# Performance work log

Hardware: AMD Instinct MI355X
Metric: run time of the kernel (lower is better)

Reference implementation:

```python
import jax, jax.numpy as jnp
import numpy as np

M = 100      # max_child_num
H = 512      # node_hidden_size == node_feat_size
E = 512      # edge_dec_hidden_size
T = 4        # edge_type_num
ITERS = 2    # num_iterations (unshared)
NUM_SEM = 57


def _lin(k, i, o, s=0.02):
    kw, kb = jax.random.split(k)
    return (jax.random.normal(kw, (i, o), jnp.float32) * s,
            jax.random.normal(kb, (o,), jnp.float32) * s)


def setup_inputs() -> dict:
    key = jax.random.key(0)
    ks = jax.random.split(key, 12)
    W_parent, b_parent = _lin(ks[0], H, H * M)
    W_exists, b_exists = _lin(ks[1], H, 1)
    W_el, b_el = _lin(ks[2], 2 * H, E)
    W_ee = jax.random.normal(ks[3], (T, E), jnp.float32) * 0.02   # stacked mlp_edge_exists
    b_ee = jax.random.normal(ks[4], (T,), jnp.float32) * 0.02
    W_ne = jax.random.normal(ks[5], (ITERS, 2 * H + E + T, H), jnp.float32) * 0.02  # per-iteration node_edge_op
    b_ne = jax.random.normal(ks[6], (ITERS, H), jnp.float32) * 0.02
    W_child, b_child = _lin(ks[7], H * (ITERS + 1), H)
    W_sem, b_sem = _lin(ks[8], H, NUM_SEM)
    W_child2, b_child2 = _lin(ks[9], H, H)
    parent_feature = jax.random.normal(ks[10], (1, H), jnp.float32)
    return dict(parent_feature=parent_feature,
                W_parent=W_parent, b_parent=b_parent,
                W_exists=W_exists, b_exists=b_exists,
                W_el=W_el, b_el=b_el,
                W_ee=W_ee, b_ee=b_ee,
                W_ne=W_ne, b_ne=b_ne,
                W_child=W_child, b_child=b_child,
                W_sem=W_sem, b_sem=b_sem,
                W_child2=W_child2, b_child2=b_child2)


def reference(parent_feature, W_parent, b_parent, W_exists, b_exists,
              W_el, b_el, W_ee, b_ee, W_ne, b_ne,
              W_child, b_child, W_sem, b_sem, W_child2, b_child2):
    # parent -> M child node features
    child = jax.nn.relu(parent_feature @ W_parent + b_parent).reshape(M, H)
    exists_logits = child @ W_exists + b_exists                     # [M,1]

    # broadcast-concat pair features -> edge latents [M,M,E]
    pair = jnp.concatenate([jnp.broadcast_to(child[:, None, :], (M, M, H)),
                            jnp.broadcast_to(child[None, :, :], (M, M, H))], -1)
    edge_latents = jax.nn.relu(pair @ W_el + b_el)                  # [M,M,E]
    edge_exists_logits = jnp.einsum('ije,te->ijt', edge_latents, W_ee) + b_ee  # [M,M,T]

    # dense edge mask == torch's nonzero(edge_exists_logits>0) filtered by node existence
    node_ok = exists_logits[:, 0] > 0
    mask = (edge_exists_logits > 0) & node_ok[:, None, None] & node_ok[None, :, None]  # [M,M,T]
    maskf = mask.astype(child.dtype)[..., None]
    any_edge = mask.any()

    # per-(i,j,t) edge feature: edge_latent concat one-hot(type)*logit
    etl = edge_exists_logits[..., None] * jnp.eye(T, dtype=child.dtype)        # [M,M,T,T]
    edge_static = jnp.concatenate(
        [jnp.broadcast_to(edge_latents[:, :, None, :], (M, M, T, E)), etl], -1)  # [M,M,T,E+T]

    feats = [child]
    for it in range(ITERS):
        ne = jnp.concatenate([
            jnp.broadcast_to(child[:, None, None, :], (M, M, T, H)),   # from-node feats (gather)
            jnp.broadcast_to(child[None, :, None, :], (M, M, T, H)),   # to-node feats (gather)
            edge_static], -1)                                          # [M,M,T,2H+E+T]
        msg = jax.nn.relu(ne @ W_ne[it] + b_ne[it]) * maskf            # [M,M,T,H]
        new_child = msg.sum(axis=(1, 2))                               # scatter_add onto 'from' index
        child = jnp.where(any_edge, new_child, child)                  # torch skips update if no edges
        feats.append(child)

    hcat = jnp.concatenate(feats, axis=1)                              # [M, H*(ITERS+1)]
    h = jax.nn.relu(hcat @ W_child + b_child)
    sem_logits = h @ W_sem + b_sem
    child_out = jax.nn.relu(h @ W_child2 + b_child2)
    return (child_out[None], sem_logits[None], exists_logits[None], edge_exists_logits[None])
```

## Files before the change

kernel.cpp:

```cpp
#include <hip/hip_runtime.h>

#define M_NODES 100
#define HDIM 512
#define MH (M_NODES*HDIM)
#define WNE_IT (1540*512)

typedef __attribute__((ext_vector_type(8))) short short8v;
typedef __attribute__((ext_vector_type(4))) float float4v;

static __device__ __forceinline__ short f2b(float f) {
    union { float f; unsigned u; } v; v.f = f;
    unsigned r = (v.u + 0x7FFF + ((v.u >> 16) & 1)) >> 16;
    return (short)r;
}

__global__ void front_kernel(const float* __restrict__ W_ne, short* __restrict__ W3t,
                             const float* __restrict__ parent, const float* __restrict__ Wp,
                             float* __restrict__ partial_c, int* __restrict__ flagjc,
                             float* __restrict__ child12) {
    __shared__ float sh[32 * 33];
    int bx = blockIdx.x, t = threadIdx.x;
    if (bx == 0 && t < 101) flagjc[t] = 0;
    if (bx < 512) {
        int it = bx >> 8, rem = bx & 255, kt = rem & 15, ht = rem >> 4;
        const float* W3 = W_ne + (size_t)it * WNE_IT + 1024 * 512;
        int tx = t & 31, ty = t >> 5;
        #pragma unroll
        for (int r = 0; r < 4; ++r) {
            int k = kt * 32 + ty * 4 + r;
            sh[(ty * 4 + r) * 33 + tx] = W3[(size_t)k * 512 + ht * 32 + tx];
        }
        __syncthreads();
        #pragma unroll
        for (int r = 0; r < 4; ++r) {
            int h = ht * 32 + ty * 4 + r;
            W3t[(size_t)it * 262144 + (size_t)h * 512 + kt * 32 + tx] = f2b(sh[tx * 33 + ty * 4 + r]);
        }
    } else if (bx < 912) {
        int b = bx - 512;
        int bxx = b % 50, byy = b / 50;
        float* p = sh;
        int kc = byy * 64;
        if (t < 64) p[t] = parent[kc + t];
        __syncthreads();
        int o4 = (bxx * 256 + t) * 4;
        float4 acc = make_float4(0.f, 0.f, 0.f, 0.f);
        #pragma unroll 4
        for (int k = 0; k < 64; ++k) {
            float4 w = *(const float4*)(Wp + (size_t)(kc + k) * MH + o4);
            float pv = p[k];
            acc.x += pv * w.x; acc.y += pv * w.y; acc.z += pv * w.z; acc.w += pv * w.w;
        }
        *(float4*)(partial_c + (size_t)byy * MH + o4) = acc;
    } else {
        int id = (bx - 912) * 256 + t;
        *(float4*)(child12 + (size_t)id * 4) = make_float4(0.f, 0.f, 0.f, 0.f);
    }
}

static __device__ __forceinline__ void ks16_tree(float4 (*red)[256], int t) {
    #pragma unroll
    for (int st = 128; st >= 16; st >>= 1) {
        if (t < st) {
            #pragma unroll
            for (int r = 0; r < 4; ++r) {
                float4 a = red[r][t], b = red[r][t + st];
                a.x += b.x; a.y += b.y; a.z += b.z; a.w += b.w;
                red[r][t] = a;
            }
        }
        __syncthreads();
    }
}

__global__ __launch_bounds__(256) void
quad_ex(const float* __restrict__ partial_c, const float* __restrict__ bp,
        const float* __restrict__ Wex, const float* __restrict__ bex,
        const float* __restrict__ B0, const float* __restrict__ B1,
        const float* __restrict__ B2, const float* __restrict__ B3,
        const float* __restrict__ bias0, const float* __restrict__ bias2,
        float* __restrict__ child0, float* __restrict__ exists_out, int* __restrict__ node_ok,
        float* __restrict__ O0, float* __restrict__ O1,
        float* __restrict__ O2, float* __restrict__ O3) {
    __shared__ float As[4][512];
    __shared__ float4 red[4][256];
    int t = threadIdx.x, bx = blockIdx.x, m0 = blockIdx.y * 4;
    #pragma unroll
    for (int q2 = 0; q2 < 2; ++q2) {
        int slot = t + q2 * 256;
        int row = slot >> 7, c4 = (slot & 127) * 4;
        int gcol = (m0 + row) * 512 + c4;
        float4 s = *(const float4*)(bp + gcol);
        #pragma unroll
        for (int q = 0; q < 8; ++q) {
            float4 v = *(const float4*)(partial_c + (size_t)q * MH + gcol);
            s.x += v.x; s.y += v.y; s.z += v.z; s.w += v.w;
        }
        s.x = fmaxf(s.x, 0.f); s.y = fmaxf(s.y, 0.f);
        s.z = fmaxf(s.z, 0.f); s.w = fmaxf(s.w, 0.f);
        *(float4*)&As[row][c4] = s;
        if (bx == 0) *(float4*)(child0 + gcol) = s;
    }
    __syncthreads();
    if (bx == 0) {
        int r = t >> 6, l = t & 63;
        const float* a = &As[r][l * 8];
        const float* w = Wex + l * 8;
        float s = a[0]*w[0] + a[1]*w[1] + a[2]*w[2] + a[3]*w[3]
                + a[4]*w[4] + a[5]*w[5] + a[6]*w[6] + a[7]*w[7];
        #pragma unroll
        for (int off = 32; off; off >>= 1) s += __shfl_down(s, off);
        if (l == 0) {
            float v = s + bex[0];
            exists_out[m0 + r] = v;
            node_ok[m0 + r] = (v > 0.f) ? 1 : 0;
        }
    }
    int kq = t >> 4, g = t & 15;
    int col4 = bx * 16 + g, which = col4 >> 7, nn4 = col4 & 127;
    const float* B = (which == 0) ? B0 : (which == 1) ? B1 : (which == 2) ? B2 : B3;
    const float* bpB = B + nn4 * 4;
    float4 a0 = {0,0,0,0}, a1 = {0,0,0,0}, a2 = {0,0,0,0}, a3 = {0,0,0,0};
    int k0 = kq * 32;
    #pragma unroll 8
    for (int i = 0; i < 32; ++i) {
        int kk = k0 + i;
        float4 b = *(const float4*)(bpB + (size_t)kk * 512);
        float x0 = As[0][kk], x1 = As[1][kk], x2 = As[2][kk], x3 = As[3][kk];
        a0.x += x0*b.x; a0.y += x0*b.y; a0.z += x0*b.z; a0.w += x0*b.w;
        a1.x += x1*b.x; a1.y += x1*b.y; a1.z += x1*b.z; a1.w += x1*b.w;
        a2.x += x2*b.x; a2.y += x2*b.y; a2.z += x2*b.z; a2.w += x2*b.w;
        a3.x += x3*b.x; a3.y += x3*b.y; a3.z += x3*b.z; a3.w += x3*b.w;
    }
    red[0][t] = a0; red[1][t] = a1; red[2][t] = a2; red[3][t] = a3;
    __syncthreads();
    ks16_tree(red, t);
    if (t < 64) {
        int r2 = t >> 4, g2 = t & 15;
        int col4b = bx * 16 + g2, which2 = col4b >> 7, nn4b = col4b & 127;
        float4 s = red[r2][g2];
        if (which2 == 0) {
            float4 bb = *(const float4*)(bias0 + nn4b * 4);
            s.x += bb.x; s.y += bb.y; s.z += bb.z; s.w += bb.w;
        } else if (which2 == 2) {
            float4 bb = *(const float4*)(bias2 + nn4b * 4);
            s.x += bb.x; s.y += bb.y; s.z += bb.z; s.w += bb.w;
        }
        float* O = (which2 == 0) ? O0 : (which2 == 1) ? O1 : (which2 == 2) ? O2 : O3;
        *(float4*)(O + (size_t)(m0 + r2) * 512 + nn4b * 4) = s;
    }
}

__global__ __launch_bounds__(256) void
dual_ab(const int* __restrict__ flagp, const float* __restrict__ A0, const float* __restrict__ A1,
        const float* __restrict__ B0, const float* __restrict__ B1,
        const float* __restrict__ bias0, float* __restrict__ O0, float* __restrict__ O1) {
    __shared__ float As[4][512];
    __shared__ float4 red[4][256];
    int t = threadIdx.x, bx = blockIdx.x, m0 = blockIdx.y * 4;
    const float* A = (*flagp) ? A1 : A0;
    #pragma unroll
    for (int q2 = 0; q2 < 2; ++q2) {
        int slot = t + q2 * 256;
        int row = slot >> 7, c4 = (slot & 127) * 4;
        *(float4*)&As[row][c4] = *(const float4*)(A + (size_t)(m0 + row) * 512 + c4);
    }
    __syncthreads();
    int kq = t >> 4, g = t & 15;
    int col4 = bx * 16 + g;
    bool second = col4 >= 128;
    const float* B = second ? B1 : B0;
    int nn4 = col4 & 127;
    const float* bpB = B + nn4 * 4;
    float4 a0 = {0,0,0,0}, a1 = {0,0,0,0}, a2 = {0,0,0,0}, a3 = {0,0,0,0};
    int k0 = kq * 32;
    #pragma unroll 8
    for (int i = 0; i < 32; ++i) {
        int kk = k0 + i;
        float4 b = *(const float4*)(bpB + (size_t)kk * 512);
        float x0 = As[0][kk], x1 = As[1][kk], x2 = As[2][kk], x3 = As[3][kk];
        a0.x += x0*b.x; a0.y += x0*b.y; a0.z += x0*b.z; a0.w += x0*b.w;
        a1.x += x1*b.x; a1.y += x1*b.y; a1.z += x1*b.z; a1.w += x1*b.w;
        a2.x += x2*b.x; a2.y += x2*b.y; a2.z += x2*b.z; a2.w += x2*b.w;
        a3.x += x3*b.x; a3.y += x3*b.y; a3.z += x3*b.z; a3.w += x3*b.w;
    }
    red[0][t] = a0; red[1][t] = a1; red[2][t] = a2; red[3][t] = a3;
    __syncthreads();
    ks16_tree(red, t);
    if (t < 64) {
        int r2 = t >> 4, g2 = t & 15;
        int col4b = bx * 16 + g2;
        bool sec2 = col4b >= 128;
        int nn4b = col4b & 127;
        float4 s = red[r2][g2];
        if (!sec2) {
            float4 bb = *(const float4*)(bias0 + nn4b * 4);
            s.x += bb.x; s.y += bb.y; s.z += bb.z; s.w += bb.w;
        }
        float* O = sec2 ? O1 : O0;
        *(float4*)(O + (size_t)(m0 + r2) * 512 + nn4b * 4) = s;
    }
}

__global__ __launch_bounds__(256) void
perm1536(const int* __restrict__ flagp, const float* __restrict__ cb,
         const float* __restrict__ B, const float* __restrict__ bias, float* __restrict__ O) {
    __shared__ float As[4][1536];
    __shared__ float4 red[4][256];
    int t = threadIdx.x, bx = blockIdx.x, m0 = blockIdx.y * 4;
    int flag = *flagp;
    #pragma unroll
    for (int q2 = 0; q2 < 6; ++q2) {
        int slot = t + q2 * 256;
        int row = slot / 384;
        int c4 = (slot - row * 384) * 4;
        int seg = c4 >> 9, off = c4 & 511;
        int se = flag ? seg : 0;
        *(float4*)&As[row][c4] = *(const float4*)(cb + (size_t)se * MH + (size_t)(m0 + row) * 512 + off);
    }
    __syncthreads();
    int kq = t >> 4, g = t & 15;
    int nn4 = bx * 16 + g;
    const float* bpB = B + nn4 * 4;
    float4 a0 = {0,0,0,0}, a1 = {0,0,0,0}, a2 = {0,0,0,0}, a3 = {0,0,0,0};
    int k0 = kq * 96;
    #pragma unroll 8
    for (int i = 0; i < 96; ++i) {
        int kk = k0 + i;
        float4 b = *(const float4*)(bpB + (size_t)kk * 512);
        float x0 = As[0][kk], x1 = As[1][kk], x2 = As[2][kk], x3 = As[3][kk];
        a0.x += x0*b.x; a0.y += x0*b.y; a0.z += x0*b.z; a0.w += x0*b.w;
        a1.x += x1*b.x; a1.y += x1*b.y; a1.z += x1*b.z; a1.w += x1*b.w;
        a2.x += x2*b.x; a2.y += x2*b.y; a2.z += x2*b.z; a2.w += x2*b.w;
        a3.x += x3*b.x; a3.y += x3*b.y; a3.z += x3*b.z; a3.w += x3*b.w;
    }
    red[0][t] = a0; red[1][t] = a1; red[2][t] = a2; red[3][t] = a3;
    __syncthreads();
    ks16_tree(red, t);
    if (t < 64) {
        int r2 = t >> 4, g2 = t & 15;
        int nn4b = bx * 16 + g2;
        float4 s = red[r2][g2];
        float4 bb = *(const float4*)(bias + nn4b * 4);
        s.x = fmaxf(s.x + bb.x, 0.f); s.y = fmaxf(s.y + bb.y, 0.f);
        s.z = fmaxf(s.z + bb.z, 0.f); s.w = fmaxf(s.w + bb.w, 0.f);
        *(float4*)(O + (size_t)(m0 + r2) * 512 + nn4b * 4) = s;
    }
}

__global__ __launch_bounds__(256) void
dual_rag(const float* __restrict__ A,
         const float* __restrict__ B0, const float* __restrict__ bias0, float* __restrict__ O0,
         const float* __restrict__ B2, const float* __restrict__ bias2, float* __restrict__ O2) {
    __shared__ float As[4][512];
    __shared__ float4 red[4][256];
    int t = threadIdx.x, bx = blockIdx.x, m0 = blockIdx.y * 4;
    #pragma unroll
    for (int q2 = 0; q2 < 2; ++q2) {
        int slot = t + q2 * 256;
        int row = slot >> 7, c4 = (slot & 127) * 4;
        *(float4*)&As[row][c4] = *(const float4*)(A + (size_t)(m0 + row) * 512 + c4);
    }
    __syncthreads();
    int kq = t >> 4, g = t & 15;
    float4 a0 = {0,0,0,0}, a1 = {0,0,0,0}, a2 = {0,0,0,0}, a3 = {0,0,0,0};
    int k0 = kq * 32;
    if (bx < 8) {
        int nn4 = bx * 16 + g;
        const float* bpB = B0 + nn4 * 4;
        #pragma unroll 8
        for (int i = 0; i < 32; ++i) {
            int kk = k0 + i;
            float4 b = *(const float4*)(bpB + (size_t)kk * 512);
            float x0 = As[0][kk], x1 = As[1][kk], x2 = As[2][kk], x3 = As[3][kk];
            a0.x += x0*b.x; a0.y += x0*b.y; a0.z += x0*b.z; a0.w += x0*b.w;
            a1.x += x1*b.x; a1.y += x1*b.y; a1.z += x1*b.z; a1.w += x1*b.w;
            a2.x += x2*b.x; a2.y += x2*b.y; a2.z += x2*b.z; a2.w += x2*b.w;
            a3.x += x3*b.x; a3.y += x3*b.y; a3.z += x3*b.z; a3.w += x3*b.w;
        }
    } else {
        int col = (bx - 8) * 16 + g;
        if (col < 57) {
            #pragma unroll 8
            for (int i = 0; i < 32; ++i) {
                int kk = k0 + i;
                float b = B2[(size_t)kk * 57 + col];
                a0.x += As[0][kk] * b; a1.x += As[1][kk] * b;
                a2.x += As[2][kk] * b; a3.x += As[3][kk] * b;
            }
        }
    }
    red[0][t] = a0; red[1][t] = a1; red[2][t] = a2; red[3][t] = a3;
    __syncthreads();
    ks16_tree(red, t);
    if (t < 64) {
        int r2 = t >> 4, g2 = t & 15;
        float4 s = red[r2][g2];
        if (bx < 8) {
            int nn4b = bx * 16 + g2;
            float4 bb = *(const float4*)(bias0 + nn4b * 4);
            s.x = fmaxf(s.x + bb.x, 0.f); s.y = fmaxf(s.y + bb.y, 0.f);
            s.z = fmaxf(s.z + bb.z, 0.f); s.w = fmaxf(s.w + bb.w, 0.f);
            *(float4*)(O0 + (size_t)(m0 + r2) * 512 + nn4b * 4) = s;
        } else {
            int col = (bx - 8) * 16 + g2;
            if (col < 57) O2[(size_t)(m0 + r2) * 57 + col] = s.x + bias2[col];
        }
    }
}

__global__ void elog_kernel(const float* __restrict__ Xi, const float* __restrict__ Xj,
                            const float* __restrict__ Wee, const float* __restrict__ bee,
                            const int* __restrict__ node_ok,
                            float* __restrict__ elog, int* __restrict__ any_flag,
                            int* __restrict__ jcount, int* __restrict__ jlist) {
    int wid = threadIdx.x >> 6, lane = threadIdx.x & 63;
    int pair = blockIdx.x * 4 + wid;
    int i = pair / M_NODES, j = pair - (pair / M_NODES) * M_NODES;
    int k0 = lane * 8;
    float4 xa = *(const float4*)(Xi + (size_t)i * HDIM + k0);
    float4 xb = *(const float4*)(Xi + (size_t)i * HDIM + k0 + 4);
    float4 ya = *(const float4*)(Xj + (size_t)j * HDIM + k0);
    float4 yb = *(const float4*)(Xj + (size_t)j * HDIM + k0 + 4);
    float e0 = fmaxf(xa.x + ya.x, 0.f), e1 = fmaxf(xa.y + ya.y, 0.f);
    float e2 = fmaxf(xa.z + ya.z, 0.f), e3 = fmaxf(xa.w + ya.w, 0.f);
    float e4 = fmaxf(xb.x + yb.x, 0.f), e5 = fmaxf(xb.y + yb.y, 0.f);
    float e6 = fmaxf(xb.z + yb.z, 0.f), e7 = fmaxf(xb.w + yb.w, 0.f);
    float s[4];
    #pragma unroll
    for (int t = 0; t < 4; ++t) {
        float4 wa = *(const float4*)(Wee + t * HDIM + k0);
        float4 wb = *(const float4*)(Wee + t * HDIM + k0 + 4);
        s[t] = e0*wa.x + e1*wa.y + e2*wa.z + e3*wa.w + e4*wb.x + e5*wb.y + e6*wb.z + e7*wb.w;
    }
    #pragma unroll
    for (int off = 32; off; off >>= 1) {
        s[0] += __shfl_down(s[0], off); s[1] += __shfl_down(s[1], off);
        s[2] += __shfl_down(s[2], off); s[3] += __shfl_down(s[3], off);
    }
    if (lane == 0) {
        bool ok = node_ok[i] && node_ok[j];
        float lg0 = s[0] + bee[0], lg1 = s[1] + bee[1], lg2 = s[2] + bee[2], lg3 = s[3] + bee[3];
        elog[pair * 4 + 0] = lg0; elog[pair * 4 + 1] = lg1;
        elog[pair * 4 + 2] = lg2; elog[pair * 4 + 3] = lg3;
        bool any = ok && (lg0 > 0.f || lg1 > 0.f || lg2 > 0.f || lg3 > 0.f);
        if (any) {
            int slot = atomicAdd(&jcount[i], 1);
            jlist[i * 112 + slot] = j;
            if (*(volatile int*)any_flag == 0) atomicOr(any_flag, 1);
        }
    }
}

__global__ __launch_bounds__(512) void
msgmfma(const float* __restrict__ Xi, const float* __restrict__ Xj,
        const float* __restrict__ Abuf, const float* __restrict__ Bbuf,
        const short* __restrict__ W3t, const float* __restrict__ W4,
        const float* __restrict__ elog, const int* __restrict__ jcount,
        const int* __restrict__ jlist, float* __restrict__ child_next) {
    __shared__ short ELb[16][520];
    __shared__ int jrow[16];
    int i = blockIdx.y;
    int jt = blockIdx.x;
    int jcnt = jcount[i];
    int j0 = jt * 16;
    if (j0 >= jcnt) return;
    int t = threadIdx.x;
    int wave = t >> 6, lane = t & 63;

    if (t < 16) jrow[t] = (j0 + t < jcnt) ? jlist[i * 112 + j0 + t] : -1;
    __syncthreads();
    int k0 = (t & 127) * 4;
    int r0 = t >> 7;
    float4 xi = *(const float4*)(Xi + (size_t)i * HDIM + k0);
    #pragma unroll
    for (int s = 0; s < 4; ++s) {
        int row = r0 + s * 4;
        int j = jrow[row];
        short4 b;
        if (j >= 0) {
            float4 xj = *(const float4*)(Xj + (size_t)j * HDIM + k0);
            b.x = f2b(fmaxf(xi.x + xj.x, 0.f));
            b.y = f2b(fmaxf(xi.y + xj.y, 0.f));
            b.z = f2b(fmaxf(xi.z + xj.z, 0.f));
            b.w = f2b(fmaxf(xi.w + xj.w, 0.f));
        } else {
            b.x = b.y = b.z = b.w = 0;
        }
        *(short4*)&ELb[row][k0] = b;
    }
    __syncthreads();

    int n = lane & 15, quad = lane >> 4;
    int h0w = wave * 64;
    float4v acc[4];
    #pragma unroll
    for (int nt = 0; nt < 4; ++nt) acc[nt] = (float4v){0.f, 0.f, 0.f, 0.f};

    for (int kc = 0; kc < 16; ++kc) {
        int koff = kc * 32 + quad * 8;
        short8v a = *(const short8v*)&ELb[n][koff];
        #pragma unroll
        for (int nt = 0; nt < 4; ++nt) {
            int hcol = h0w + nt * 16 + n;
            short8v b = *(const short8v*)(W3t + (size_t)hcol * 512 + koff);
            acc[nt] = __builtin_amdgcn_mfma_f32_16x16x32_bf16(a, b, acc[nt], 0, 0, 0);
        }
    }

    #pragma unroll
    for (int nt = 0; nt < 4; ++nt) {
        int hcol = h0w + nt * 16 + n;
        float aval = Abuf[(size_t)i * HDIM + hcol];
        float w40 = W4[hcol], w41 = W4[HDIM + hcol], w42 = W4[2*HDIM + hcol], w43 = W4[3*HDIM + hcol];
        float s = 0.f;
        #pragma unroll
        for (int reg = 0; reg < 4; ++reg) {
            int jj = jrow[quad * 4 + reg];
            if (jj >= 0) {
                float s0 = aval + Bbuf[(size_t)jj * HDIM + hcol] + acc[nt][reg];
                const float* lgp = elog + ((size_t)i * M_NODES + jj) * 4;
                float lg;
                lg = lgp[0]; if (lg > 0.f) s += fmaxf(s0 + lg * w40, 0.f);
                lg = lgp[1]; if (lg > 0.f) s += fmaxf(s0 + lg * w41, 0.f);
                lg = lgp[2]; if (lg > 0.f) s += fmaxf(s0 + lg * w42, 0.f);
                lg = lgp[3]; if (lg > 0.f) s += fmaxf(s0 + lg * w43, 0.f);
            }
        }
        s += __shfl_xor(s, 16);
        s += __shfl_xor(s, 32);
        if (lane < 16) atomicAdd(&child_next[(size_t)i * HDIM + hcol], s);
    }
}

extern "C" void kernel_launch(void* const* d_in, const int* in_sizes, int n_in,
                              void* d_out, int out_size, void* d_ws, size_t ws_size,
                              hipStream_t stream) {
    const float* parent   = (const float*)d_in[0];
    const float* W_parent = (const float*)d_in[1];
    const float* b_parent = (const float*)d_in[2];
    const float* W_exists = (const float*)d_in[3];
    const float* b_exists = (const float*)d_in[4];
    const float* W_el     = (const float*)d_in[5];
    const float* b_el     = (const float*)d_in[6];
    const float* W_ee     = (const float*)d_in[7];
    const float* b_ee     = (const float*)d_in[8];
    const float* W_ne     = (const float*)d_in[9];
    const float* b_ne     = (const float*)d_in[10];
    const float* W_child  = (const float*)d_in[11];
    const float* b_child  = (const float*)d_in[12];
    const float* W_sem    = (const float*)d_in[13];
    const float* b_sem    = (const float*)d_in[14];
    const float* W_child2 = (const float*)d_in[15];
    const float* b_child2 = (const float*)d_in[16];
    float* out = (float*)d_out;

    float* ws = (float*)d_ws;
    float* child_bufs = ws;
    float* Xi       = ws + 3 * MH;
    float* Xj       = Xi + MH;
    float* Abuf     = Xj + MH;
    float* Bbuf     = Abuf + MH;
    int*   node_ok  = (int*)(Bbuf + MH);
    int*   flag     = node_ok + M_NODES;
    int*   jcount   = flag + 1;
    int*   jlist    = jcount + 100;
    float* scratch  = (float*)(jlist + 11200 + 3);
    short* W3t      = (short*)(scratch + 8 * MH);
    float* hbuf     = Xi;

    float* out_child  = out;
    float* out_sem    = out + 51200;
    float* out_exists = out + 56900;
    float* out_elog   = out + 57000;

    front_kernel<<<1012, 256, 0, stream>>>(W_ne, W3t, parent, W_parent, scratch, flag,
                                           child_bufs + MH);

    quad_ex<<<dim3(32, 25), 256, 0, stream>>>(scratch, b_parent, W_exists, b_exists,
        W_el, W_el + 512 * 512, W_ne, W_ne + 512 * 512, b_el, b_ne,
        child_bufs, out_exists, node_ok, Xi, Xj, Abuf, Bbuf);

    elog_kernel<<<2500, 256, 0, stream>>>(Xi, Xj, W_ee, b_ee, node_ok, out_elog, flag,
                                          jcount, jlist);

    msgmfma<<<dim3(7, M_NODES), 512, 0, stream>>>(Xi, Xj, Abuf, Bbuf,
        W3t, W_ne + 1536 * 512, out_elog, jcount, jlist, child_bufs + MH);

    dual_ab<<<dim3(16, 25), 256, 0, stream>>>(flag, child_bufs, child_bufs + MH,
        W_ne + WNE_IT, W_ne + WNE_IT + 512 * 512, b_ne + 512, Abuf, Bbuf);

    msgmfma<<<dim3(7, M_NODES), 512, 0, stream>>>(Xi, Xj, Abuf, Bbuf,
        W3t + 262144, W_ne + WNE_IT + 1536 * 512, out_elog, jcount, jlist,
        child_bufs + 2 * MH);

    perm1536<<<dim3(8, 25), 256, 0, stream>>>(flag, child_bufs, W_child, b_child, hbuf);

    dual_rag<<<dim3(12, 25), 256, 0, stream>>>(hbuf, W_child2, b_child2, out_child,
                                               W_sem, b_sem, out_sem);
}
```

Before: 340.8 us.

## Process four pairs per wave in elog and split msgmfma H across two blocks

elog_kernel now has each wave handle four consecutive j pairs, so the W_ee weight vectors and the Xi row are loaded once and reused, and the grid shrinks fourfold. msgmfma drops to 256 threads per block and splits the 512 hidden columns across two blocks via blockIdx.x, doubling the grid to give more, smaller blocks. The cost is that each msgmfma block rebuilds the same 16-row edge-latent tile in shared memory, so that staging work is duplicated.

```diff
diff --git a/kernel.cpp b/kernel.cpp
--- a/kernel.cpp
+++ b/kernel.cpp
@@ -315,44 +315,55 @@
                             float* __restrict__ elog, int* __restrict__ any_flag,
                             int* __restrict__ jcount, int* __restrict__ jlist) {
     int wid = threadIdx.x >> 6, lane = threadIdx.x & 63;
-    int pair = blockIdx.x * 4 + wid;
-    int i = pair / M_NODES, j = pair - (pair / M_NODES) * M_NODES;
+    int pair0 = (blockIdx.x * 4 + wid) * 4;
+    int i = pair0 / M_NODES, j0 = pair0 - i * M_NODES;
     int k0 = lane * 8;
     float4 xa = *(const float4*)(Xi + (size_t)i * HDIM + k0);
     float4 xb = *(const float4*)(Xi + (size_t)i * HDIM + k0 + 4);
-    float4 ya = *(const float4*)(Xj + (size_t)j * HDIM + k0);
-    float4 yb = *(const float4*)(Xj + (size_t)j * HDIM + k0 + 4);
-    float e0 = fmaxf(xa.x + ya.x, 0.f), e1 = fmaxf(xa.y + ya.y, 0.f);
-    float e2 = fmaxf(xa.z + ya.z, 0.f), e3 = fmaxf(xa.w + ya.w, 0.f);
-    float e4 = fmaxf(xb.x + yb.x, 0.f), e5 = fmaxf(xb.y + yb.y, 0.f);
-    float e6 = fmaxf(xb.z + yb.z, 0.f), e7 = fmaxf(xb.w + yb.w, 0.f);
-    float s[4];
-    #pragma unroll
-    for (int t = 0; t < 4; ++t) {
-        float4 wa = *(const float4*)(Wee + t * HDIM + k0);
-        float4 wb = *(const float4*)(Wee + t * HDIM + k0 + 4);
-        s[t] = e0*wa.x + e1*wa.y + e2*wa.z + e3*wa.w + e4*wb.x + e5*wb.y + e6*wb.z + e7*wb.w;
-    }
-    #pragma unroll
-    for (int off = 32; off; off >>= 1) {
-        s[0] += __shfl_down(s[0], off); s[1] += __shfl_down(s[1], off);
-        s[2] += __shfl_down(s[2], off); s[3] += __shfl_down(s[3], off);
-    }
-    if (lane == 0) {
-        bool ok = node_ok[i] && node_ok[j];
-        float lg0 = s[0] + bee[0], lg1 = s[1] + bee[1], lg2 = s[2] + bee[2], lg3 = s[3] + bee[3];
-        elog[pair * 4 + 0] = lg0; elog[pair * 4 + 1] = lg1;
-        elog[pair * 4 + 2] = lg2; elog[pair * 4 + 3] = lg3;
-        bool any = ok && (lg0 > 0.f || lg1 > 0.f || lg2 > 0.f || lg3 > 0.f);
-        if (any) {
-            int slot = atomicAdd(&jcount[i], 1);
-            jlist[i * 112 + slot] = j;
-            if (*(volatile int*)any_flag == 0) atomicOr(any_flag, 1);
-        }
-    }
-}
-
-__global__ __launch_bounds__(512) void
+    float4 wa[4], wb[4];
+    #pragma unroll
+    for (int tt = 0; tt < 4; ++tt) {
+        wa[tt] = *(const float4*)(Wee + tt * HDIM + k0);
+        wb[tt] = *(const float4*)(Wee + tt * HDIM + k0 + 4);
+    }
+    int oki = node_ok[i];
+    for (int jj = 0; jj < 4; ++jj) {
+        int j = j0 + jj;
+        float4 ya = *(const float4*)(Xj + (size_t)j * HDIM + k0);
+        float4 yb = *(const float4*)(Xj + (size_t)j * HDIM + k0 + 4);
+        float e0 = fmaxf(xa.x + ya.x, 0.f), e1 = fmaxf(xa.y + ya.y, 0.f);
+        float e2 = fmaxf(xa.z + ya.z, 0.f), e3 = fmaxf(xa.w + ya.w, 0.f);
+        float e4 = fmaxf(xb.x + yb.x, 0.f), e5 = fmaxf(xb.y + yb.y, 0.f);
+        float e6 = fmaxf(xb.z + yb.z, 0.f), e7 = fmaxf(xb.w + yb.w, 0.f);
+        float s[4];
+        #pragma unroll
+        for (int tt = 0; tt < 4; ++tt) {
+            s[tt] = e0*wa[tt].x + e1*wa[tt].y + e2*wa[tt].z + e3*wa[tt].w
+                  + e4*wb[tt].x + e5*wb[tt].y + e6*wb[tt].z + e7*wb[tt].w;
+        }
+        #pragma unroll
+        for (int off = 32; off; off >>= 1) {
+            s[0] += __shfl_down(s[0], off); s[1] += __shfl_down(s[1], off);
+            s[2] += __shfl_down(s[2], off); s[3] += __shfl_down(s[3], off);
+        }
+        if (lane == 0) {
+            int pair = pair0 + jj;
+            bool ok = oki && node_ok[j];
+            float lg0 = s[0] + bee[0], lg1 = s[1] + bee[1];
+            float lg2 = s[2] + bee[2], lg3 = s[3] + bee[3];
+            elog[pair * 4 + 0] = lg0; elog[pair * 4 + 1] = lg1;
+            elog[pair * 4 + 2] = lg2; elog[pair * 4 + 3] = lg3;
+            bool any = ok && (lg0 > 0.f || lg1 > 0.f || lg2 > 0.f || lg3 > 0.f);
+            if (any) {
+                int slot = atomicAdd(&jcount[i], 1);
+                jlist[i * 112 + slot] = j;
+                if (*(volatile int*)any_flag == 0) atomicOr(any_flag, 1);
+            }
+        }
+    }
+}
+
+__global__ __launch_bounds__(256) void
 msgmfma(const float* __restrict__ Xi, const float* __restrict__ Xj,
         const float* __restrict__ Abuf, const float* __restrict__ Bbuf,
         const short* __restrict__ W3t, const float* __restrict__ W4,
@@ -361,7 +372,7 @@
     __shared__ short ELb[16][520];
     __shared__ int jrow[16];
     int i = blockIdx.y;
-    int jt = blockIdx.x;
+    int jt = blockIdx.x >> 1, hs = blockIdx.x & 1;
     int jcnt = jcount[i];
     int j0 = jt * 16;
     if (j0 >= jcnt) return;
@@ -374,8 +385,8 @@
     int r0 = t >> 7;
     float4 xi = *(const float4*)(Xi + (size_t)i * HDIM + k0);
     #pragma unroll
-    for (int s = 0; s < 4; ++s) {
-        int row = r0 + s * 4;
+    for (int s = 0; s < 8; ++s) {
+        int row = r0 + s * 2;
         int j = jrow[row];
         short4 b;
         if (j >= 0) {
@@ -392,7 +403,7 @@
     __syncthreads();
 
     int n = lane & 15, quad = lane >> 4;
-    int h0w = wave * 64;
+    int h0w = hs * 256 + wave * 64;
     float4v acc[4];
     #pragma unroll
     for (int nt = 0; nt < 4; ++nt) acc[nt] = (float4v){0.f, 0.f, 0.f, 0.f};
@@ -481,16 +492,16 @@
         W_el, W_el + 512 * 512, W_ne, W_ne + 512 * 512, b_el, b_ne,
         child_bufs, out_exists, node_ok, Xi, Xj, Abuf, Bbuf);
 
-    elog_kernel<<<2500, 256, 0, stream>>>(Xi, Xj, W_ee, b_ee, node_ok, out_elog, flag,
-                                          jcount, jlist);
-
-    msgmfma<<<dim3(7, M_NODES), 512, 0, stream>>>(Xi, Xj, Abuf, Bbuf,
+    elog_kernel<<<625, 256, 0, stream>>>(Xi, Xj, W_ee, b_ee, node_ok, out_elog, flag,
+                                         jcount, jlist);
+
+    msgmfma<<<dim3(14, M_NODES), 256, 0, stream>>>(Xi, Xj, Abuf, Bbuf,
         W3t, W_ne + 1536 * 512, out_elog, jcount, jlist, child_bufs + MH);
 
     dual_ab<<<dim3(16, 25), 256, 0, stream>>>(flag, child_bufs, child_bufs + MH,
         W_ne + WNE_IT, W_ne + WNE_IT + 512 * 512, b_ne + 512, Abuf, Bbuf);
 
-    msgmfma<<<dim3(7, M_NODES), 512, 0, stream>>>(Xi, Xj, Abuf, Bbuf,
+    msgmfma<<<dim3(14, M_NODES), 256, 0, stream>>>(Xi, Xj, Abuf, Bbuf,
         W3t + 262144, W_ne + WNE_IT + 1536 * 512, out_elog, jcount, jlist,
         child_bufs + 2 * MH);
 
```

After: 360.6 us. +5.8%, slower.

## Replace atomic edge-list build with ballot compaction and split message blocks by hidden half

Applied to the files above, without the earlier changes.

The edge-logit kernel now writes a per-pair existence byte instead of appending to per-row lists with atomics. A new compaction kernel builds each row's ordered neighbor list with wave ballots and popcounts. The message kernel is split into two blocks of 256 threads, each covering half the hidden columns, so twice as many smaller blocks are launched. This removes atomic contention and gives deterministic list order, at the cost of an extra launch and duplicated edge-latent staging in each half-block.

```diff
diff --git a/kernel.cpp b/kernel.cpp
--- a/kernel.cpp
+++ b/kernel.cpp
@@ -312,8 +312,7 @@
 __global__ void elog_kernel(const float* __restrict__ Xi, const float* __restrict__ Xj,
                             const float* __restrict__ Wee, const float* __restrict__ bee,
                             const int* __restrict__ node_ok,
-                            float* __restrict__ elog, int* __restrict__ any_flag,
-                            int* __restrict__ jcount, int* __restrict__ jlist) {
+                            float* __restrict__ elog, int* __restrict__ anyb) {
     int wid = threadIdx.x >> 6, lane = threadIdx.x & 63;
     int pair = blockIdx.x * 4 + wid;
     int i = pair / M_NODES, j = pair - (pair / M_NODES) * M_NODES;
@@ -328,10 +327,10 @@
     float e6 = fmaxf(xb.z + yb.z, 0.f), e7 = fmaxf(xb.w + yb.w, 0.f);
     float s[4];
     #pragma unroll
-    for (int t = 0; t < 4; ++t) {
-        float4 wa = *(const float4*)(Wee + t * HDIM + k0);
-        float4 wb = *(const float4*)(Wee + t * HDIM + k0 + 4);
-        s[t] = e0*wa.x + e1*wa.y + e2*wa.z + e3*wa.w + e4*wb.x + e5*wb.y + e6*wb.z + e7*wb.w;
+    for (int tt = 0; tt < 4; ++tt) {
+        float4 wa = *(const float4*)(Wee + tt * HDIM + k0);
+        float4 wb = *(const float4*)(Wee + tt * HDIM + k0 + 4);
+        s[tt] = e0*wa.x + e1*wa.y + e2*wa.z + e3*wa.w + e4*wb.x + e5*wb.y + e6*wb.z + e7*wb.w;
     }
     #pragma unroll
     for (int off = 32; off; off >>= 1) {
@@ -343,16 +342,31 @@
         float lg0 = s[0] + bee[0], lg1 = s[1] + bee[1], lg2 = s[2] + bee[2], lg3 = s[3] + bee[3];
         elog[pair * 4 + 0] = lg0; elog[pair * 4 + 1] = lg1;
         elog[pair * 4 + 2] = lg2; elog[pair * 4 + 3] = lg3;
-        bool any = ok && (lg0 > 0.f || lg1 > 0.f || lg2 > 0.f || lg3 > 0.f);
-        if (any) {
-            int slot = atomicAdd(&jcount[i], 1);
-            jlist[i * 112 + slot] = j;
-            if (*(volatile int*)any_flag == 0) atomicOr(any_flag, 1);
-        }
-    }
-}
-
-__global__ __launch_bounds__(512) void
+        anyb[pair] = (ok && (lg0 > 0.f || lg1 > 0.f || lg2 > 0.f || lg3 > 0.f)) ? 1 : 0;
+    }
+}
+
+__global__ void compact_kernel(const int* __restrict__ anyb, int* __restrict__ jcount,
+                               int* __restrict__ jlist, int* __restrict__ flag) {
+    int wid = threadIdx.x >> 6, lane = threadIdx.x & 63;
+    int i = blockIdx.x * 4 + wid;
+    const int* ab = anyb + i * M_NODES;
+    bool b0 = ab[lane] != 0;
+    bool b1 = (lane < 36) ? (ab[64 + lane] != 0) : false;
+    unsigned long long m0 = __ballot(b0);
+    unsigned long long m1 = __ballot(b1);
+    int c0 = __popcll(m0);
+    int cnt = c0 + __popcll(m1);
+    unsigned long long below = (lane == 0) ? 0ull : (~0ull >> (64 - lane));
+    if (b0) jlist[i * 112 + __popcll(m0 & below)] = lane;
+    if (b1) jlist[i * 112 + c0 + __popcll(m1 & below)] = 64 + lane;
+    if (lane == 0) {
+        jcount[i] = cnt;
+        if (cnt > 0) atomicOr(flag, 1);
+    }
+}
+
+__global__ __launch_bounds__(256) void
 msgmfma(const float* __restrict__ Xi, const float* __restrict__ Xj,
         const float* __restrict__ Abuf, const float* __restrict__ Bbuf,
         const short* __restrict__ W3t, const float* __restrict__ W4,
@@ -361,7 +375,7 @@
     __shared__ short ELb[16][520];
     __shared__ int jrow[16];
     int i = blockIdx.y;
-    int jt = blockIdx.x;
+    int jt = blockIdx.x >> 1, hs = blockIdx.x & 1;
     int jcnt = jcount[i];
     int j0 = jt * 16;
     if (j0 >= jcnt) return;
@@ -374,8 +388,8 @@
     int r0 = t >> 7;
     float4 xi = *(const float4*)(Xi + (size_t)i * HDIM + k0);
     #pragma unroll
-    for (int s = 0; s < 4; ++s) {
-        int row = r0 + s * 4;
+    for (int s = 0; s < 8; ++s) {
+        int row = r0 + s * 2;
         int j = jrow[row];
         short4 b;
         if (j >= 0) {
@@ -392,7 +406,7 @@
     __syncthreads();
 
     int n = lane & 15, quad = lane >> 4;
-    int h0w = wave * 64;
+    int h0w = hs * 256 + wave * 64;
     float4v acc[4];
     #pragma unroll
     for (int nt = 0; nt < 4; ++nt) acc[nt] = (float4v){0.f, 0.f, 0.f, 0.f};
@@ -465,7 +479,8 @@
     int*   flag     = node_ok + M_NODES;
     int*   jcount   = flag + 1;
     int*   jlist    = jcount + 100;
-    float* scratch  = (float*)(jlist + 11200 + 3);
+    int*   anyb     = jlist + 11200;
+    float* scratch  = (float*)(anyb + 10000 + 7);
     short* W3t      = (short*)(scratch + 8 * MH);
     float* hbuf     = Xi;
 
@@ -481,16 +496,17 @@
         W_el, W_el + 512 * 512, W_ne, W_ne + 512 * 512, b_el, b_ne,
         child_bufs, out_exists, node_ok, Xi, Xj, Abuf, Bbuf);
 
-    elog_kernel<<<2500, 256, 0, stream>>>(Xi, Xj, W_ee, b_ee, node_ok, out_elog, flag,
-                                          jcount, jlist);
-
-    msgmfma<<<dim3(7, M_NODES), 512, 0, stream>>>(Xi, Xj, Abuf, Bbuf,
+    elog_kernel<<<2500, 256, 0, stream>>>(Xi, Xj, W_ee, b_ee, node_ok, out_elog, anyb);
+
+    compact_kernel<<<25, 256, 0, stream>>>(anyb, jcount, jlist, flag);
+
+    msgmfma<<<dim3(14, M_NODES), 256, 0, stream>>>(Xi, Xj, Abuf, Bbuf,
         W3t, W_ne + 1536 * 512, out_elog, jcount, jlist, child_bufs + MH);
 
     dual_ab<<<dim3(16, 25), 256, 0, stream>>>(flag, child_bufs, child_bufs + MH,
         W_ne + WNE_IT, W_ne + WNE_IT + 512 * 512, b_ne + 512, Abuf, Bbuf);
 
-    msgmfma<<<dim3(7, M_NODES), 512, 0, stream>>>(Xi, Xj, Abuf, Bbuf,
+    msgmfma<<<dim3(14, M_NODES), 256, 0, stream>>>(Xi, Xj, Abuf, Bbuf,
         W3t + 262144, W_ne + WNE_IT + 1536 * 512, out_elog, jcount, jlist,
         child_bufs + 2 * MH);
 
```

Result: faster. 312.9 us (-8.2%).
